# Optimization experiments

Measured on AMD Instinct MI355X. Metric: run time of the kernel, lower is better.

The kernel has to match this reference:

```python
import jax, jax.numpy as jnp
import numpy as np

B, S, H, W, C = 2, 21, 256, 256, 256
Q, NEG = 256, 256
TEMP = 0.5
STRONG_T = 1.0
EPS = 1e-8


def setup_inputs():
    key = jax.random.key(0)
    k1, k2, k3 = jax.random.split(key, 3)
    rep = jax.random.normal(k1, (B, C, H, W), jnp.float32)
    label = jax.random.randint(k2, (B, 1, H, W), 0, S)
    mask = jnp.ones((B, 1, H, W), jnp.float32)
    prob = jax.random.uniform(k3, (B, S, H, W), jnp.float32)
    return {"rep": rep, "label": label, "mask": mask, "prob": prob}


def _cos(a, b, axis=-1):
    # torch.cosine_similarity: dot / (max(|a|,eps) * max(|b|,eps))
    an = jnp.maximum(jnp.linalg.norm(a, axis=axis), EPS)
    bn = jnp.maximum(jnp.linalg.norm(b, axis=axis), EPS)
    return jnp.sum(a * b, axis=axis) / (an * bn)


def _reco_loss(rep, label, mask, prob):
    Sg = prob.shape[1]
    Cf = rep.shape[1]
    lab = label.reshape(-1).astype(jnp.int32)          # [N]
    ignore = lab > Sg - 1
    lab = jnp.where(ignore, 0, lab)
    m = jnp.where(ignore, 0.0, mask.reshape(-1))
    valid = m > 0                                      # [N]
    feats = jnp.transpose(rep, (0, 2, 3, 1)).reshape(-1, Cf)   # [N,C]
    pflat = jnp.transpose(prob, (0, 2, 3, 1)).reshape(-1, Sg)  # [N,S]
    p_lab = jnp.take_along_axis(pflat, lab[:, None], axis=1)[:, 0]
    hard = valid & (p_lab < STRONG_T)

    seg_id = jnp.where(valid, lab, Sg)  # invalid pixels -> overflow bucket Sg
    counts = jax.ops.segment_sum(valid.astype(jnp.int32), seg_id, num_segments=Sg + 1)[:Sg]
    hard_counts = jax.ops.segment_sum(hard.astype(jnp.int32), seg_id, num_segments=Sg + 1)[:Sg]
    proto = jax.ops.segment_sum(feats * valid[:, None].astype(feats.dtype), seg_id,
                                num_segments=Sg + 1)[:Sg]
    proto = proto / jnp.maximum(counts, 1)[:, None].astype(feats.dtype)  # [S,C]

    # stable sort pixels by (segment, hard-first): emulates the per-segment
    # boolean-mask gathers / concatenation order of the torch code
    order = jnp.argsort(seg_id * 2 + (~hard).astype(jnp.int32))
    feats_sorted = feats[order]                                 # [N,C]
    off = jnp.concatenate([jnp.zeros((1,), counts.dtype), jnp.cumsum(counts)[:-1]])

    seg_ids = jnp.arange(Sg)
    keys = jax.random.split(jax.random.key(1), Sg)

    def body(acc, xs):
        i, ki = xs
        ka, kc, kn = jax.random.split(ki, 3)
        # anchors: num_queries random hard pixels of segment i
        hidx = off[i] + jax.random.randint(ka, (Q,), 0, jnp.maximum(hard_counts[i], 1))
        anchor = feats_sorted[hidx]                             # [Q,C]
        # negative class distribution over other segments (rolled order)
        roll = (i + 1 + jnp.arange(Sg - 1)) % Sg
        proto_logits = _cos(proto[i][None, :], proto[roll]) / TEMP  # [S-1]
        samp = jax.random.categorical(kc, proto_logits, shape=(Q, NEG))
        neg_seg = roll[samp]                                    # [Q,NEG]
        # uniform pixel within each sampled segment's block
        u = jax.random.uniform(kn, (Q, NEG))
        nidx = off[neg_seg] + jnp.floor(u * jnp.maximum(counts[neg_seg], 1)).astype(counts.dtype)
        neg_feat = feats_sorted[nidx]                           # [Q,NEG,C]
        all_feat = jnp.concatenate(
            [jnp.broadcast_to(proto[i], (Q, 1, Cf)), neg_feat], axis=1)
        all_feat = jax.lax.stop_gradient(all_feat)              # torch.no_grad block
        seg_logits = _cos(anchor[:, None, :], all_feat) / TEMP  # [Q,1+NEG]
        # cross-entropy with target 0, mean over queries
        ce = jnp.mean(jax.nn.logsumexp(seg_logits, axis=1) - seg_logits[:, 0])
        acc = acc + jnp.where(hard_counts[i] > 0, ce, 0.0)
        return acc, None

    total, _ = jax.lax.scan(body, jnp.float32(0.0), (seg_ids, keys))
    valid_seg = jnp.sum(counts > 0)
    loss = total / jnp.maximum(valid_seg, 1).astype(jnp.float32)
    return jnp.where(valid_seg > 1, loss, jnp.float32(0.0))


def reference(rep, label, mask, prob):
    loss_weight = 1.0
    return loss_weight * _reco_loss(rep, label, mask, prob)
```

## Files before the change

### kernel.cpp

```cpp
#include <hip/hip_runtime.h>
#include <stdint.h>

#define NPIX  131072
#define HW    65536
#define CCH   256
#define NSEG  21
#define NROLL 20

typedef float f32x2 __attribute__((ext_vector_type(2)));
typedef __fp16 half2t __attribute__((ext_vector_type(2)));

__device__ __forceinline__ uint64_t rng64(uint32_t i, uint32_t q, uint32_t j) {
  uint64_t x = ((uint64_t)((i << 8) | q) << 32) | (uint64_t)(j * 0x9E3779B1u);
  x ^= 0xD1B54A32D192ED03ULL;
  x += 0x9E3779B97F4A7C15ULL;
  x = (x ^ (x >> 30)) * 0xBF58476D1CE4E5B9ULL;
  x = (x ^ (x >> 27)) * 0x94D049BB133111EBULL;
  return x ^ (x >> 31);
}

__device__ __forceinline__ float fdot2h(half2t a, half2t b, float c) {
  return __builtin_amdgcn_fdot2(a, b, c, false);
}

__device__ __forceinline__ void dec16(uint4 w, half2t* nx) {
  uint32_t dw[4] = { w.x, w.y, w.z, w.w };
#pragma unroll
  for (int d = 0; d < 4; ++d) {
    f32x2 lo = __builtin_amdgcn_cvt_pk_f32_fp8((int)dw[d], false);
    f32x2 hi = __builtin_amdgcn_cvt_pk_f32_fp8((int)dw[d], true);
    nx[d * 2 + 0] = __builtin_amdgcn_cvt_pkrtz(lo.x, lo.y);
    nx[d * 2 + 1] = __builtin_amdgcn_cvt_pkrtz(hi.x, hi.y);
  }
}

__global__ __launch_bounds__(256) void reco_a(
    const float* __restrict__ rep, const int* __restrict__ label,
    const float* __restrict__ mask, const float* __restrict__ prob,
    uint8_t* __restrict__ f8, float* __restrict__ norms,
    int* __restrict__ labh, int* __restrict__ bc, float4* __restrict__ zr) {
  int t = threadIdx.x;
  __shared__ __align__(16) char SM[68352];

  if (blockIdx.x < 2048) {
    float* tile = (float*)SM;
    float* partial = (float*)(SM + 65792);
    float* inv = (float*)(SM + 66816);
    int bid = blockIdx.x;
    int wtile = bid & 3;
    int row = bid >> 2;
    int b = row >> 8, h = row & 255;
    int w0 = wtile * 64;

    const float* repb = rep + (size_t)b * CCH * HW + (size_t)h * 256 + w0;
    int w4 = t & 15, cbase = t >> 4;
#pragma unroll
    for (int it = 0; it < 16; ++it) {
      int c = it * 16 + cbase;
      float4 v = *(const float4*)&repb[(size_t)c * HW + w4 * 4];
      tile[(w4 * 4 + 0) * 257 + c] = v.x;
      tile[(w4 * 4 + 1) * 257 + c] = v.y;
      tile[(w4 * 4 + 2) * 257 + c] = v.z;
      tile[(w4 * 4 + 3) * 257 + c] = v.w;
    }
    __syncthreads();
    {
      int w = t & 63, qtr = t >> 6;
      float acc = 0.f;
#pragma unroll 8
      for (int cc = 0; cc < 64; ++cc) {
        float v = tile[w * 257 + qtr * 64 + cc];
        acc += v * v;
      }
      partial[qtr * 64 + w] = acc;
    }
    __syncthreads();
    if (t < 64) {
      float s = partial[0 * 64 + t] + partial[1 * 64 + t] + partial[2 * 64 + t] + partial[3 * 64 + t];
      float nm = fmaxf(sqrtf(s), 1e-8f);
      inv[t] = 1.0f / nm;
      norms[row * 256 + w0 + t] = nm;
    }
    __syncthreads();
    int pix = t & 7, chunk = t >> 3;
#pragma unroll
    for (int it = 0; it < 8; ++it) {
      int p = it * 8 + pix;
      float iv = inv[p];
      float v[8];
#pragma unroll
      for (int k = 0; k < 8; ++k) v[k] = tile[p * 257 + chunk * 8 + k] * iv;
      uint32_t lo = 0, hi = 0;
      lo = (uint32_t)__builtin_amdgcn_cvt_pk_fp8_f32(v[0], v[1], (int)lo, false);
      lo = (uint32_t)__builtin_amdgcn_cvt_pk_fp8_f32(v[2], v[3], (int)lo, true);
      hi = (uint32_t)__builtin_amdgcn_cvt_pk_fp8_f32(v[4], v[5], (int)hi, false);
      hi = (uint32_t)__builtin_amdgcn_cvt_pk_fp8_f32(v[6], v[7], (int)hi, true);
      size_t n = (size_t)(row * 256 + w0 + p);
      uint2 o; o.x = lo; o.y = hi;
      *(uint2*)&f8[n * CCH + chunk * 8] = o;
    }
  } else {
    int row = blockIdx.x - 2048;
    int b = row >> 8, h = row & 255;
    int n = row * 256 + t;
    if (row < 6) {
      int idx = row * 256 + t;
      if (idx < 1360) zr[idx] = make_float4(0.f, 0.f, 0.f, 0.f);
    }
    int lab = label[n];
    bool ignore = lab > NSEG - 1;
    if (ignore) lab = 0;
    float mval = ignore ? 0.f : mask[n];
    bool valid = mval > 0.f;
    float p_lab = prob[(((size_t)b * NSEG + lab) * 256 + h) * 256 + t];
    bool hard = valid && (p_lab < 1.0f);
    labh[n] = lab | (hard ? 32 : 0) | (valid ? 64 : 0);

    int* cpart = (int*)SM;
    int* hpart = (int*)SM + 24;
    if (t < NSEG) { cpart[t] = 0; hpart[t] = 0; }
    __syncthreads();
    if (valid) { atomicAdd(&cpart[lab], 1); if (hard) atomicAdd(&hpart[lab], 1); }
    __syncthreads();
    if (t < NSEG) {
      bc[t * 512 + row] = cpart[t];
      bc[(24 + t) * 512 + row] = hpart[t];
    }
  }
}

__global__ __launch_bounds__(256) void reco_k2t(
    const int* __restrict__ bc, int* __restrict__ counts, int* __restrict__ hardc,
    int* __restrict__ offs, int* __restrict__ cur_h, int* __restrict__ cur_e) {
  int t = threadIdx.x;
  int wave = t >> 6, lane = t & 63;
  __shared__ int sums[42];
  for (int c = wave; c < 42; c += 4) {
    int col = (c < 21) ? c : c + 3;
    const int* p = bc + col * 512 + lane * 8;
    int s = 0;
#pragma unroll
    for (int j = 0; j < 8; ++j) s += p[j];
#pragma unroll
    for (int o = 32; o >= 1; o >>= 1) s += __shfl_xor(s, o);
    if (lane == 0) sums[c] = s;
  }
  __syncthreads();
  if (t == 0) {
    int o = 0;
    for (int s = 0; s < NSEG; ++s) {
      counts[s] = sums[s];
      hardc[s] = sums[21 + s];
      offs[s] = o;
      cur_h[s] = o;
      cur_e[s] = o + sums[21 + s];
      o += sums[s];
    }
    offs[NSEG] = o;
  }
}

__global__ __launch_bounds__(256) void reco_k3(const int* __restrict__ labh,
                        int* __restrict__ cur_h, int* __restrict__ cur_e, int* __restrict__ list) {
  int t = threadIdx.x;
  int n = blockIdx.x * 256 + t;
  __shared__ int lcnt[2 * NSEG];
  __shared__ int lbase[2 * NSEG];
  if (t < 2 * NSEG) lcnt[t] = 0;
  __syncthreads();
  int v = labh[n];
  int lab = v & 31;
  bool hard = (v & 32) != 0;
  bool valid = (v & 64) != 0;
  int bucket = lab + (hard ? 0 : NSEG);
  int rank = 0;
  if (valid) rank = atomicAdd(&lcnt[bucket], 1);
  __syncthreads();
  if (t < 2 * NSEG) {
    int c = lcnt[t];
    lbase[t] = c ? atomicAdd((t < NSEG) ? &cur_h[t] : &cur_e[t - NSEG], c) : 0;
  }
  __syncthreads();
  if (valid) list[lbase[bucket] + rank] = n;
}

__global__ __launch_bounds__(256) void reco_proto8(
    const uint8_t* __restrict__ f8, const float* __restrict__ norms,
    const int* __restrict__ list, const int* __restrict__ labh,
    const int* __restrict__ offs, float* __restrict__ proto) {
  int t = threadIdx.x;
  int base = blockIdx.x * 256;
  int total = offs[NSEG];

  __shared__ uint8_t rows[64][256];
  __shared__ float nrm[64];
  __shared__ int segs[256];
  __shared__ int pixs[256];
  __shared__ float red[64][17];

  {
    int pos = base + t;
    int p = (pos < total) ? (list[pos] & (NPIX - 1)) : -1;
    pixs[t] = p;
    segs[t] = (p >= 0) ? (labh[p] & 31) : -1;
  }
  __syncthreads();

  int d = t & 63, qt = t >> 6;
  float a0 = 0.f, a1 = 0.f, a2 = 0.f, a3 = 0.f;
  int cseg = -2;

  for (int sub = 0; sub < 4; ++sub) {
    {
      int r = t >> 2, c = (t & 3) * 64;
      int p = pixs[sub * 64 + r];
      uint4* dst = (uint4*)&rows[r][c];
      if (p >= 0) {
        const uint4* src = (const uint4*)&f8[(size_t)p * CCH + c];
        dst[0] = src[0]; dst[1] = src[1]; dst[2] = src[2]; dst[3] = src[3];
      } else {
        uint4 z = make_uint4(0, 0, 0, 0);
        dst[0] = z; dst[1] = z; dst[2] = z; dst[3] = z;
      }
      if (t < 64) {
        int pp = pixs[sub * 64 + t];
        nrm[t] = (pp >= 0) ? norms[pp] : 0.f;
      }
    }
    __syncthreads();
    for (int pp = 0; pp < 16; ++pp) {
      int pl = qt * 16 + pp;
      int sg = segs[sub * 64 + pl];
      if (sg >= 0) {
        if (sg != cseg) {
          if (cseg >= 0) {
            atomicAdd(&proto[cseg * CCH + d * 4 + 0], a0);
            atomicAdd(&proto[cseg * CCH + d * 4 + 1], a1);
            atomicAdd(&proto[cseg * CCH + d * 4 + 2], a2);
            atomicAdd(&proto[cseg * CCH + d * 4 + 3], a3);
          }
          a0 = a1 = a2 = a3 = 0.f;
          cseg = sg;
        }
        uint32_t w = *(const uint32_t*)&rows[pl][d * 4];
        f32x2 lo = __builtin_amdgcn_cvt_pk_f32_fp8((int)w, false);
        f32x2 hi = __builtin_amdgcn_cvt_pk_f32_fp8((int)w, true);
        float nv = nrm[pl];
        a0 += lo.x * nv; a1 += lo.y * nv; a2 += hi.x * nv; a3 += hi.y * nv;
      }
    }
    __syncthreads();
  }

  int s0 = segs[0];
  int uni = __syncthreads_and((cseg < 0) || (cseg == s0));
  if (uni) {
    if (cseg >= 0) {
      red[d][qt * 4 + 0] = a0;
      red[d][qt * 4 + 1] = a1;
      red[d][qt * 4 + 2] = a2;
      red[d][qt * 4 + 3] = a3;
    }
    __syncthreads();
    if (t < 64 && s0 >= 0) {
#pragma unroll
      for (int c = 0; c < 4; ++c) {
        float v = red[t][0 + c] + red[t][4 + c] + red[t][8 + c] + red[t][12 + c];
        atomicAdd(&proto[s0 * CCH + t * 4 + c], v);
      }
    }
  } else if (cseg >= 0) {
    atomicAdd(&proto[cseg * CCH + d * 4 + 0], a0);
    atomicAdd(&proto[cseg * CCH + d * 4 + 1], a1);
    atomicAdd(&proto[cseg * CCH + d * 4 + 2], a2);
    atomicAdd(&proto[cseg * CCH + d * 4 + 3], a3);
  }
}

__global__ __launch_bounds__(256) void reco_k6r(
    const uint8_t* __restrict__ f8, const int* __restrict__ list,
    const int* __restrict__ counts, const int* __restrict__ hardc,
    const int* __restrict__ offs, const float* __restrict__ proto,
    float* __restrict__ seg_sum, int* __restrict__ ticket, float* __restrict__ out) {
  int bid = blockIdx.x;
  int i  = bid >> 5;
  int qc = bid & 31;
  int t = threadIdx.x;

  __shared__ float spN[NSEG * CCH];
  __shared__ float pn[NSEG];
  __shared__ float lgrow[NROLL];
  __shared__ half2t anch[8 * 128];
  __shared__ float lgts[8][264];
  __shared__ float s_cdf[NROLL];
  __shared__ int s_off[NSEG], s_cnt[NSEG], s_pidx[256], s_apix[8];
  __shared__ float s_ce[8];
  __shared__ int s_last;

  if (t < NSEG) { s_off[t] = offs[t]; s_cnt[t] = counts[t]; }
  __syncthreads();

  for (int idx = t; idx < NSEG * CCH; idx += 256) {
    int s = idx >> 8;
    int c = s_cnt[s]; if (c < 1) c = 1;
    spN[idx] = proto[idx] / (float)c;
  }
  __syncthreads();
  if (t < NSEG) {
    float s2 = 0.f;
    for (int c = 0; c < CCH; ++c) { float v = spN[t * CCH + c]; s2 += v * v; }
    pn[t] = fmaxf(sqrtf(s2), 1e-8f);
  }
  __syncthreads();
  for (int idx = t; idx < NSEG * CCH; idx += 256) {
    int s = idx >> 8;
    spN[idx] = spN[idx] / pn[s];
  }
  __syncthreads();
  if (t < NROLL) {
    int j = (i + 1 + t) % NSEG;
    float d = 0.f;
    for (int c = 0; c < CCH; ++c) d += spN[i * CCH + c] * spN[j * CCH + c];
    lgrow[t] = d * 2.0f;
  }
  __syncthreads();
  if (t == 0) {
    float mx = -1e30f;
    for (int k = 0; k < NROLL; ++k) mx = fmaxf(mx, lgrow[k]);
    float e[NROLL]; float s = 0.f;
    for (int k = 0; k < NROLL; ++k) { e[k] = __expf(lgrow[k] - mx); s += e[k]; }
    float a = 0.f;
    for (int k = 0; k < NROLL; ++k) { a += e[k] / s; s_cdf[k] = a; }
    s_cdf[NROLL - 1] = 2.0f;
  }
  if (t < 8) {
    int q = qc * 8 + t;
    uint64_t r = rng64(i, q, 511u);
    int hc = hardc[i]; if (hc < 1) hc = 1;
    uint32_t jj = (uint32_t)(r & 0xffffffffu) % (uint32_t)hc;
    int idx = offs[i] + (int)jj;
    if (idx > NPIX - 1) idx = NPIX - 1;
    s_apix[t] = list[idx] & (NPIX - 1);
  }
  __syncthreads();

  {
    uint64_t r = rng64(i, 0u, (uint32_t)(t + 1));
    float u1 = (float)(r >> 40) * (1.0f / 16777216.0f);
    float u2 = (float)((r >> 16) & 0xFFFFFFu) * (1.0f / 16777216.0f);
    int k = 0;
#pragma unroll
    for (int kk = 0; kk < NROLL - 1; ++kk) k += (u1 >= s_cdf[kk]);
    int seg = i + 1 + k; if (seg >= NSEG) seg -= NSEG;
    int cnt = s_cnt[seg]; int cm = cnt < 1 ? 1 : cnt;
    int pidx = (int)(u2 * (float)cm);
    if (pidx > cm - 1) pidx = cm - 1;
    int li = s_off[seg] + pidx;
    if (li > NPIX - 1) li = NPIX - 1;
    s_pidx[t] = list[li] & (NPIX - 1);
  }
  if (t < 128) {
    int g = t >> 4, x = t & 15;
    uint4 w = *(const uint4*)&f8[(size_t)s_apix[g] * CCH + x * 16];
    half2t dx[8]; dec16(w, dx);
#pragma unroll
    for (int k = 0; k < 8; ++k) anch[g * 128 + x * 8 + k] = dx[k];
  }
  __syncthreads();

  const uint4* rowp = (const uint4*)&f8[(size_t)s_pidx[t] * CCH];
  float acc[8];
#pragma unroll
  for (int q = 0; q < 8; ++q) acc[q] = 0.f;
  for (int k0 = 0; k0 < 16; k0 += 4) {
    uint4 w4[4];
#pragma unroll
    for (int u = 0; u < 4; ++u) w4[u] = rowp[k0 + u];
#pragma unroll
    for (int u = 0; u < 4; ++u) {
      half2t nx[8]; dec16(w4[u], nx);
      const half2t* ar = anch + (k0 + u) * 8;
#pragma unroll
      for (int q = 0; q < 8; ++q) {
        const half2t* a = ar + q * 128;
        float s = acc[q];
#pragma unroll
        for (int k = 0; k < 8; ++k) s = fdot2h(a[k], nx[k], s);
        acc[q] = s;
      }
    }
  }
  float ps = 0.f;
  if (t < 128) {
    int g = t >> 4, x = t & 15;
    const float* pNs = spN + i * CCH;
#pragma unroll
    for (int k = 0; k < 8; ++k) {
      half2t a = anch[g * 128 + x * 8 + k];
      ps += (float)a.x * pNs[x * 16 + 2 * k] + (float)a.y * pNs[x * 16 + 2 * k + 1];
    }
#pragma unroll
    for (int o = 1; o <= 8; o <<= 1) ps += __shfl_xor(ps, o);
  }

#pragma unroll
  for (int q = 0; q < 8; ++q) lgts[q][1 + t] = acc[q] * 2.0f;
  if (t < 128 && (t & 15) == 0) lgts[t >> 4][0] = ps * 2.0f;
  __syncthreads();

  int wave = t >> 6, lane = t & 63;
  for (int q = wave; q < 8; q += 4) {
    const float* L = lgts[q];
    float v0 = L[lane], v1 = L[lane + 64], v2 = L[lane + 128], v3 = L[lane + 192];
    float v4 = (lane == 0) ? L[256] : -1e30f;
    float m = fmaxf(fmaxf(fmaxf(v0, v1), fmaxf(v2, v3)), v4);
#pragma unroll
    for (int o = 32; o >= 1; o >>= 1) m = fmaxf(m, __shfl_xor(m, o));
    float e = __expf(v0 - m) + __expf(v1 - m) + __expf(v2 - m) + __expf(v3 - m)
            + ((lane == 0) ? __expf(v4 - m) : 0.f);
#pragma unroll
    for (int o = 32; o >= 1; o >>= 1) e += __shfl_xor(e, o);
    if (lane == 0) s_ce[q] = m + logf(e) - L[0];
  }
  __syncthreads();
  if (t == 0) {
    float s = 0.f;
#pragma unroll
    for (int q = 0; q < 8; ++q) s += s_ce[q];
    atomicAdd(&seg_sum[i], s);
    __threadfence();
    int done = atomicAdd(ticket, 1);
    s_last = (done == NSEG * 32 - 1);
  }
  __syncthreads();
  if (s_last && t == 0) {
    __threadfence();
    float tot = 0.f; int vs = 0;
    for (int s = 0; s < NSEG; ++s) {
      vs += (counts[s] > 0);
      float v = atomicAdd(&seg_sum[s], 0.f);
      if (hardc[s] > 0) tot += v;
    }
    float loss = (tot * (1.0f / 256.0f)) / (float)(vs > 0 ? vs : 1);
    out[0] = (vs > 1) ? loss : 0.f;
  }
}

extern "C" void kernel_launch(void* const* d_in, const int* in_sizes, int n_in,
                              void* d_out, int out_size, void* d_ws, size_t ws_size,
                              hipStream_t stream) {
  const float* rep   = (const float*)d_in[0];
  const int*   label = (const int*)d_in[1];
  const float* mask  = (const float*)d_in[2];
  const float* prob  = (const float*)d_in[3];

  char* ws = (char*)d_ws;
  uint8_t* f8 = (uint8_t*)ws;
  size_t o = 67108864;
  float* norms  = (float*)(ws + o); o += 524288;
  int*   list   = (int*)(ws + o);   o += 524288;
  int*   labh   = (int*)(ws + o);   o += 524288;
  float* proto  = (float*)(ws + o); o += 21504;
  float* segsum = (float*)(ws + o); o += 128;
  int*   ticket = (int*)(ws + o);   o += 128;
  int*   counts = (int*)(ws + o);   o += 128;
  int*   hardc  = (int*)(ws + o);   o += 128;
  int*   offs   = (int*)(ws + o);   o += 128;
  int*   cur_h  = (int*)(ws + o);   o += 128;
  int*   cur_e  = (int*)(ws + o);   o += 128;
  int*   bc     = (int*)(ws + o);   o += 98304;

  reco_a<<<2560, 256, 0, stream>>>(rep, label, mask, prob, f8, norms, labh, bc, (float4*)proto);
  reco_k2t<<<1, 256, 0, stream>>>(bc, counts, hardc, offs, cur_h, cur_e);
  reco_k3<<<512, 256, 0, stream>>>(labh, cur_h, cur_e, list);
  reco_proto8<<<512, 256, 0, stream>>>(f8, norms, list, labh, offs, proto);
  reco_k6r<<<NSEG * 32, 256, 0, stream>>>(f8, list, counts, hardc, offs, proto,
                                          segsum, ticket, (float*)d_out);
}
```

Measured before the change: 106.6 us.

## Halve transpose tile width in reco_a to raise occupancy and widen fp8 stores

The fp32-to-fp8 transpose/normalize stage now processes 32 pixels per block instead of 64. This halves shared memory per block and doubles the block count, so more blocks fit per CU and more loads are in flight. The fp8 output stage also writes 16-byte stores covering 32 channels per thread instead of 8-byte stores. Global reads per channel row shrink to 128 bytes, which may lower coalescing efficiency, and the norm reduction now sums 8 partials instead of 4.

Result: no change. 105.5 us, median of 2 (-1.0%).

```diff
diff --git a/kernel.cpp b/kernel.cpp
--- a/kernel.cpp
+++ b/kernel.cpp
@@ -34,29 +34,34 @@
   }
 }
 
+__device__ __forceinline__ uint32_t pack4fp8(float a, float b, float c, float d) {
+  uint32_t w = 0;
+  w = (uint32_t)__builtin_amdgcn_cvt_pk_fp8_f32(a, b, (int)w, false);
+  w = (uint32_t)__builtin_amdgcn_cvt_pk_fp8_f32(c, d, (int)w, true);
+  return w;
+}
+
 __global__ __launch_bounds__(256) void reco_a(
     const float* __restrict__ rep, const int* __restrict__ label,
     const float* __restrict__ mask, const float* __restrict__ prob,
     uint8_t* __restrict__ f8, float* __restrict__ norms,
     int* __restrict__ labh, int* __restrict__ bc, float4* __restrict__ zr) {
   int t = threadIdx.x;
-  __shared__ __align__(16) char SM[68352];
-
-  if (blockIdx.x < 2048) {
+  __shared__ __align__(16) char SM[34048];
+
+  if (blockIdx.x < 4096) {
     float* tile = (float*)SM;
-    float* partial = (float*)(SM + 65792);
-    float* inv = (float*)(SM + 66816);
+    float* partial = (float*)(SM + 32896);
+    float* inv = (float*)(SM + 33920);
     int bid = blockIdx.x;
-    int wtile = bid & 3;
-    int row = bid >> 2;
+    int row = bid >> 3;
+    int w0 = (bid & 7) * 32;
     int b = row >> 8, h = row & 255;
-    int w0 = wtile * 64;
-
     const float* repb = rep + (size_t)b * CCH * HW + (size_t)h * 256 + w0;
-    int w4 = t & 15, cbase = t >> 4;
-#pragma unroll
-    for (int it = 0; it < 16; ++it) {
-      int c = it * 16 + cbase;
+    int w4 = t & 7, cbase = t >> 3;
+#pragma unroll
+    for (int it = 0; it < 8; ++it) {
+      int c = it * 32 + cbase;
       float4 v = *(const float4*)&repb[(size_t)c * HW + w4 * 4];
       tile[(w4 * 4 + 0) * 257 + c] = v.x;
       tile[(w4 * 4 + 1) * 257 + c] = v.y;
@@ -65,42 +70,45 @@
     }
     __syncthreads();
     {
-      int w = t & 63, qtr = t >> 6;
+      int w = t & 31, qtr = t >> 5;
       float acc = 0.f;
 #pragma unroll 8
-      for (int cc = 0; cc < 64; ++cc) {
-        float v = tile[w * 257 + qtr * 64 + cc];
+      for (int cc = 0; cc < 32; ++cc) {
+        float v = tile[w * 257 + qtr * 32 + cc];
         acc += v * v;
       }
-      partial[qtr * 64 + w] = acc;
-    }
-    __syncthreads();
-    if (t < 64) {
-      float s = partial[0 * 64 + t] + partial[1 * 64 + t] + partial[2 * 64 + t] + partial[3 * 64 + t];
+      partial[qtr * 32 + w] = acc;
+    }
+    __syncthreads();
+    if (t < 32) {
+      float s = 0.f;
+#pragma unroll
+      for (int j = 0; j < 8; ++j) s += partial[j * 32 + t];
       float nm = fmaxf(sqrtf(s), 1e-8f);
       inv[t] = 1.0f / nm;
       norms[row * 256 + w0 + t] = nm;
     }
     __syncthreads();
-    int pix = t & 7, chunk = t >> 3;
-#pragma unroll
-    for (int it = 0; it < 8; ++it) {
-      int p = it * 8 + pix;
-      float iv = inv[p];
-      float v[8];
-#pragma unroll
-      for (int k = 0; k < 8; ++k) v[k] = tile[p * 257 + chunk * 8 + k] * iv;
-      uint32_t lo = 0, hi = 0;
-      lo = (uint32_t)__builtin_amdgcn_cvt_pk_fp8_f32(v[0], v[1], (int)lo, false);
-      lo = (uint32_t)__builtin_amdgcn_cvt_pk_fp8_f32(v[2], v[3], (int)lo, true);
-      hi = (uint32_t)__builtin_amdgcn_cvt_pk_fp8_f32(v[4], v[5], (int)hi, false);
-      hi = (uint32_t)__builtin_amdgcn_cvt_pk_fp8_f32(v[6], v[7], (int)hi, true);
-      size_t n = (size_t)(row * 256 + w0 + p);
-      uint2 o; o.x = lo; o.y = hi;
-      *(uint2*)&f8[n * CCH + chunk * 8] = o;
+    {
+      int px = t & 31, chunk = t >> 5;
+      float iv = inv[px];
+      size_t n = (size_t)(row * 256 + w0 + px);
+#pragma unroll
+      for (int hk = 0; hk < 2; ++hk) {
+        float v[16];
+#pragma unroll
+        for (int k = 0; k < 16; ++k)
+          v[k] = tile[px * 257 + chunk * 32 + hk * 16 + k] * iv;
+        uint4 o;
+        o.x = pack4fp8(v[0], v[1], v[2], v[3]);
+        o.y = pack4fp8(v[4], v[5], v[6], v[7]);
+        o.z = pack4fp8(v[8], v[9], v[10], v[11]);
+        o.w = pack4fp8(v[12], v[13], v[14], v[15]);
+        *(uint4*)&f8[n * CCH + chunk * 32 + hk * 16] = o;
+      }
     }
   } else {
-    int row = blockIdx.x - 2048;
+    int row = blockIdx.x - 4096;
     int b = row >> 8, h = row & 255;
     int n = row * 256 + t;
     if (row < 6) {
@@ -470,7 +478,8 @@
   int*   cur_e  = (int*)(ws + o);   o += 128;
   int*   bc     = (int*)(ws + o);   o += 98304;
 
-  reco_a<<<2560, 256, 0, stream>>>(rep, label, mask, prob, f8, norms, labh, bc, (float4*)proto);
+  reco_a<<<4608, 256, 0, stream>>>(rep, label, mask, prob, f8, norms, labh, bc,
+                                   (float4*)proto);
   reco_k2t<<<1, 256, 0, stream>>>(bc, counts, hardc, offs, cur_h, cur_e);
   reco_k3<<<512, 256, 0, stream>>>(labh, cur_h, cur_e, list);
   reco_proto8<<<512, 256, 0, stream>>>(f8, norms, list, labh, offs, proto);
```
